# Kernel optimization log

Hardware: AMD Instinct MI355X
Metric: run time of the kernel (lower is better)

## Reference

```python
import jax, jax.numpy as jnp
import numpy as np

NUM_EMBEDDINGS = 512
EMBEDDING_DIM = 64
COMMITMENT_COST = 0.25


def setup_inputs() -> dict:
    key = jax.random.key(0)
    k1, k2 = jax.random.split(key)
    inputs = jax.random.normal(k1, (128, 1024, EMBEDDING_DIM), dtype=jnp.float32)
    embedding = jax.random.normal(k2, (NUM_EMBEDDINGS, EMBEDDING_DIM), dtype=jnp.float32)
    return {"inputs": inputs, "embedding": embedding}


def reference(inputs, embedding):
    """Eval-mode forward of VectorQuantizerEMA.

    Returns (loss, quantized, perplexity, encodings), matching the torch module
    with self.training == False.
    """
    input_shape = inputs.shape
    flat = inputs.reshape(-1, EMBEDDING_DIM)                      # [N, D]
    distances = (
        jnp.sum(flat ** 2, axis=1, keepdims=True)
        + jnp.sum(embedding ** 2, axis=1)
        - 2.0 * flat @ embedding.T
    )
    encoding_indices = jnp.argmin(distances, axis=1)              # [N]
    encodings = jax.nn.one_hot(encoding_indices, NUM_EMBEDDINGS, dtype=jnp.float32)  # [N, K]
    # quantized = onehot @ W  ==  gather rows (same math, cheaper)
    quantized = jnp.take(embedding, encoding_indices, axis=0).reshape(input_shape)

    e_latent_loss = jnp.mean((jax.lax.stop_gradient(quantized) - inputs) ** 2)
    loss = COMMITMENT_COST * e_latent_loss

    # straight-through estimator
    quantized = inputs + jax.lax.stop_gradient(quantized - inputs)

    avg_probs = jnp.mean(encodings, axis=0)                       # [K]
    perplexity = jnp.exp(-jnp.sum(avg_probs * jnp.log(avg_probs + 1e-10)))
    return loss, quantized, perplexity, encodings
```

## Files before the change

kernel.cpp:

```cpp
#include <hip/hip_runtime.h>
#include <math.h>


#define NK 512
#define ND 64
#define NROWS 131072
#define ROWS_PB 64
#define BLOCK 256
#define NBLOCKS (NROWS / ROWS_PB)
#define NTILES 32
#define XSTRIDE 68
#define MARGIN 0.02f

#define Q_OFF    1
#define PERP_OFF 8388609
#define ENC_OFF  8388610

typedef float vf2 __attribute__((ext_vector_type(2)));
typedef float vf4 __attribute__((ext_vector_type(4)));
typedef short vs8 __attribute__((ext_vector_type(8)));

__device__ __forceinline__ unsigned short bf16_rne(float v) {
    union { float f; unsigned int u; } a; a.f = v;
    return (unsigned short)((a.u + 0x7FFFu + ((a.u >> 16) & 1u)) >> 16);
}
__device__ __forceinline__ float bf16_to_f(unsigned short s) {
    union { unsigned int u; float f; } a; a.u = ((unsigned int)s) << 16;
    return a.f;
}

__global__ __launch_bounds__(64) void vq_prep(const float* __restrict__ emb,
                                              float* __restrict__ eknorm,
                                              unsigned int* __restrict__ efrag) {
    const int t = blockIdx.x;
    const int l = threadIdx.x;
    const int c = t * 16 + (l & 15);
    const int quad = l >> 4;
    #pragma unroll
    for (int f = 0; f < 4; ++f) {
        const int kbase = (f & 1) * 32 + quad * 8;
        unsigned int w[4];
        #pragma unroll
        for (int d = 0; d < 4; ++d) {
            float v0 = emb[c * ND + kbase + 2 * d];
            float v1 = emb[c * ND + kbase + 2 * d + 1];
            unsigned short h0 = bf16_rne(v0), h1 = bf16_rne(v1);
            unsigned short l0 = bf16_rne(v0 - bf16_to_f(h0));
            unsigned short l1 = bf16_rne(v1 - bf16_to_f(h1));
            unsigned short e0 = (f < 2) ? h0 : l0;
            unsigned short e1 = (f < 2) ? h1 : l1;
            w[d] = (unsigned int)e0 | ((unsigned int)e1 << 16);
        }
        unsigned int* dst = efrag + ((size_t)(t * 4 + f) * 64 + l) * 4;
        dst[0] = w[0]; dst[1] = w[1]; dst[2] = w[2]; dst[3] = w[3];
    }
    if (quad == 0) {
        const vf4* er = (const vf4*)(emb + c * ND);
        float s0 = 0.f, s1 = 0.f, s2 = 0.f, s3 = 0.f;
        #pragma unroll
        for (int j = 0; j < 16; ++j) {
            vf4 v = er[j];
            s0 += v.x * v.x; s1 += v.y * v.y; s2 += v.z * v.z; s3 += v.w * v.w;
        }
        eknorm[c] = (s0 + s1) + (s2 + s3);
    }
}

__global__ __launch_bounds__(BLOCK) void vq_main(const float* __restrict__ x,
                                                 const float* __restrict__ emb,
                                                 const float* __restrict__ eknorm,
                                                 const unsigned int* __restrict__ efrag,
                                                 float* __restrict__ out,
                                                 int* __restrict__ g_counts,
                                                 float* __restrict__ g_loss) {
    __shared__ float lds_x[ROWS_PB * XSTRIDE];
    __shared__ float ek_lds[NK];
    __shared__ float d1s[ROWS_PB], d2s[ROWS_PB];
    __shared__ int   i1s[ROWS_PB], i2s[ROWS_PB];
    __shared__ int   idx_s[ROWS_PB];
    __shared__ float red[4];

    const int tid  = threadIdx.x;
    const int wave = tid >> 6;
    const int lane = tid & 63;
    const int col  = lane & 15;
    const int quad = lane >> 4;

    {
        const vf4* xp = (const vf4*)(x + (size_t)blockIdx.x * ROWS_PB * ND);
        #pragma unroll
        for (int i = 0; i < 4; ++i) {
            int e4 = tid + i * BLOCK;
            int r  = e4 >> 4;
            int c4 = (e4 & 15) * 4;
            *(vf4*)&lds_x[r * XSTRIDE + c4] = xp[e4];
        }
        ek_lds[tid] = eknorm[tid];
        ek_lds[tid + 256] = eknorm[tid + 256];
    }
    __syncthreads();

    const int arow = wave * 16 + col;
    vs8 ah0, ah1, al0, al1;
    {
        const float* xr = &lds_x[arow * XSTRIDE];
        #pragma unroll
        for (int j = 0; j < 8; ++j) {
            float va = xr[quad * 8 + j];
            float vb = xr[32 + quad * 8 + j];
            unsigned short ha = bf16_rne(va);
            unsigned short hb = bf16_rne(vb);
            ah0[j] = (short)ha; al0[j] = (short)bf16_rne(va - bf16_to_f(ha));
            ah1[j] = (short)hb; al1[j] = (short)bf16_rne(vb - bf16_to_f(hb));
        }
    }

    float d1[4], d2[4];
    int   i1[4], i2[4];
    #pragma unroll
    for (int r = 0; r < 4; ++r) { d1[r] = INFINITY; d2[r] = INFINITY; i1[r] = 0x7FFFFFFF; i2[r] = 0x7FFFFFFF; }

    const vs8* bbase = (const vs8*)efrag;
    vs8 b0 = bbase[(0 * 4 + 0) * 64 + lane];
    vs8 b1 = bbase[(0 * 4 + 1) * 64 + lane];
    vs8 b2 = bbase[(0 * 4 + 2) * 64 + lane];
    vs8 b3 = bbase[(0 * 4 + 3) * 64 + lane];

    for (int t = 0; t < NTILES; ++t) {
        vs8 n0, n1, n2, n3;
        if (t + 1 < NTILES) {
            n0 = bbase[((t + 1) * 4 + 0) * 64 + lane];
            n1 = bbase[((t + 1) * 4 + 1) * 64 + lane];
            n2 = bbase[((t + 1) * 4 + 2) * 64 + lane];
            n3 = bbase[((t + 1) * 4 + 3) * 64 + lane];
        }
        vf4 acc = {0.f, 0.f, 0.f, 0.f};
        acc = __builtin_amdgcn_mfma_f32_16x16x32_bf16(ah0, b0, acc, 0, 0, 0);
        acc = __builtin_amdgcn_mfma_f32_16x16x32_bf16(ah1, b1, acc, 0, 0, 0);
        acc = __builtin_amdgcn_mfma_f32_16x16x32_bf16(al0, b0, acc, 0, 0, 0);
        acc = __builtin_amdgcn_mfma_f32_16x16x32_bf16(al1, b1, acc, 0, 0, 0);
        acc = __builtin_amdgcn_mfma_f32_16x16x32_bf16(ah0, b2, acc, 0, 0, 0);
        acc = __builtin_amdgcn_mfma_f32_16x16x32_bf16(ah1, b3, acc, 0, 0, 0);
        acc = __builtin_amdgcn_mfma_f32_16x16x32_bf16(al0, b2, acc, 0, 0, 0);
        acc = __builtin_amdgcn_mfma_f32_16x16x32_bf16(al1, b3, acc, 0, 0, 0);

        const float ek = ek_lds[t * 16 + col];
        const int cidx = t * 16 + col;
        #pragma unroll
        for (int r = 0; r < 4; ++r) {
            float d = ek - 2.f * acc[r];
            bool lt1 = d < d1[r];
            bool lt2 = d < d2[r];
            float nd2 = lt1 ? d1[r] : (lt2 ? d : d2[r]);
            int   ni2 = lt1 ? i1[r] : (lt2 ? cidx : i2[r]);
            d2[r] = nd2; i2[r] = ni2;
            d1[r] = lt1 ? d : d1[r];
            i1[r] = lt1 ? cidx : i1[r];
        }
        b0 = n0; b1 = n1; b2 = n2; b3 = n3;
    }

    #pragma unroll
    for (int m = 8; m >= 1; m >>= 1) {
        #pragma unroll
        for (int r = 0; r < 4; ++r) {
            float od1 = __shfl_xor(d1[r], m);
            int   oi1 = __shfl_xor(i1[r], m);
            float od2 = __shfl_xor(d2[r], m);
            int   oi2 = __shfl_xor(i2[r], m);
            bool aF = (d1[r] < od1) || (d1[r] == od1 && i1[r] < oi1);
            float n1 = aF ? d1[r] : od1;  int ni1 = aF ? i1[r] : oi1;
            float ca = aF ? od1 : d1[r];  int cia = aF ? oi1 : i1[r];
            float cb = aF ? d2[r] : od2;  int cib = aF ? i2[r] : oi2;
            bool bF = (cb < ca) || (cb == ca && cib < cia);
            float n2 = bF ? cb : ca;      int ni2 = bF ? cib : cia;
            d1[r] = n1; i1[r] = ni1; d2[r] = n2; i2[r] = ni2;
        }
    }
    if (col == 0) {
        #pragma unroll
        for (int r = 0; r < 4; ++r) {
            int lr = wave * 16 + quad * 4 + r;
            d1s[lr] = d1[r]; i1s[lr] = i1[r];
            d2s[lr] = d2[r]; i2s[lr] = i2[r];
        }
    }
    __syncthreads();

    if (tid < ROWS_PB) {
        int am = i1s[tid];
        if (d2s[tid] - d1s[tid] < MARGIN) {
            int ia = i1s[tid], ib = i2s[tid];
            const float* xr = &lds_x[tid * XSTRIDE];
            float da, db;
            {
                const vf4* er = (const vf4*)(emb + ia * ND);
                float s0 = 0.f, s1 = 0.f, s2 = 0.f, s3 = 0.f;
                #pragma unroll
                for (int j = 0; j < 16; ++j) {
                    vf4 v = er[j];
                    s0 += xr[4 * j] * v.x; s1 += xr[4 * j + 1] * v.y;
                    s2 += xr[4 * j + 2] * v.z; s3 += xr[4 * j + 3] * v.w;
                }
                da = ek_lds[ia] - 2.f * ((s0 + s1) + (s2 + s3));
            }
            {
                const vf4* er = (const vf4*)(emb + ib * ND);
                float s0 = 0.f, s1 = 0.f, s2 = 0.f, s3 = 0.f;
                #pragma unroll
                for (int j = 0; j < 16; ++j) {
                    vf4 v = er[j];
                    s0 += xr[4 * j] * v.x; s1 += xr[4 * j + 1] * v.y;
                    s2 += xr[4 * j + 2] * v.z; s3 += xr[4 * j + 3] * v.w;
                }
                db = ek_lds[ib] - 2.f * ((s0 + s1) + (s2 + s3));
            }
            am = ((db < da) || (db == da && ib < ia)) ? ib : ia;
        }
        idx_s[tid] = am;
        atomicAdd(&g_counts[am], 1);
    }
    __syncthreads();

    float lacc = 0.f;
    {
        float* qout = out + Q_OFF + (size_t)blockIdx.x * ROWS_PB * ND;
        #pragma unroll 4
        for (int i = 0; i < 16; ++i) {
            int p = tid + i * BLOCK;
            int r = p >> 6;
            int c = p & 63;
            float q = emb[idx_s[r] * ND + c];
            float xv = lds_x[r * XSTRIDE + c];
            qout[p] = q;
            float dlt = q - xv;
            lacc += dlt * dlt;
        }
    }
    #pragma unroll
    for (int off = 32; off >= 1; off >>= 1) lacc += __shfl_down(lacc, off);
    if (lane == 0) red[wave] = lacc;
    __syncthreads();
    if (tid == 0) atomicAdd(g_loss, (red[0] + red[1]) + (red[2] + red[3]));

    {
        vf2* eout = (vf2*)(out + ENC_OFF) + (size_t)blockIdx.x * ROWS_PB * NK / 2;
        #pragma unroll 4
        for (int i = 0; i < 64; ++i) {
            int p = tid + i * BLOCK;
            int r = p >> 8;
            int c2 = p & 255;
            int am = idx_s[r];
            vf2 v = {0.f, 0.f};
            if ((am >> 1) == c2) {
                if (am & 1) v.y = 1.f; else v.x = 1.f;
            }
            __builtin_nontemporal_store(v, &eout[p]);
        }
    }
}

__global__ __launch_bounds__(512) void vq_final(const int* __restrict__ g_counts,
                                                const float* __restrict__ g_loss,
                                                float* __restrict__ out) {
    __shared__ float red[8];
    int t = threadIdx.x;
    float p = (float)g_counts[t] * (1.0f / (float)NROWS);
    float h = p * logf(p + 1e-10f);
    #pragma unroll
    for (int off = 32; off >= 1; off >>= 1) h += __shfl_down(h, off);
    if ((t & 63) == 0) red[t >> 6] = h;
    __syncthreads();
    if (t == 0) {
        float s = 0.f;
        #pragma unroll
        for (int i = 0; i < 8; ++i) s += red[i];
        out[PERP_OFF] = expf(-s);
        out[0] = 0.25f * g_loss[0] / (float)(NROWS * ND);
    }
}

extern "C" void kernel_launch(void* const* d_in, const int* in_sizes, int n_in,
                              void* d_out, int out_size, void* d_ws, size_t ws_size,
                              hipStream_t stream) {
    const float* x   = (const float*)d_in[0];
    const float* emb = (const float*)d_in[1];
    float* out = (float*)d_out;

    int*          g_counts = (int*)d_ws;
    float*        g_loss   = (float*)((char*)d_ws + 2048);
    float*        eknorm   = (float*)((char*)d_ws + 4096);
    unsigned int* efrag    = (unsigned int*)((char*)d_ws + 8192);

    (void)hipMemsetAsync(d_ws, 0, 4096, stream);

    vq_prep<<<NTILES, 64, 0, stream>>>(emb, eknorm, efrag);
    vq_main<<<NBLOCKS, BLOCK, 0, stream>>>(x, emb, eknorm, efrag, out, g_counts, g_loss);
    vq_final<<<1, 512, 0, stream>>>(g_counts, g_loss, out);
}
```

Before: 372.9 us.

## Zero-fill encodings with aligned vector stores, scatter ones, drop lo×lo MFMA terms

The one-hot encodings output is now written as a bulk zero-fill of 16-byte nontemporal stores. Two 8-byte edge stores handle the misaligned output offset. After a barrier, each row's 1.0 is written in a single scatter, replacing the per-element compare-and-store loop with 8-byte stores. The distance MFMA chain drops the two low×low correction products and splits the rest over two accumulators to shorten the dependency chain. Quantized stores also become nontemporal. The precision loss from the dropped terms relies on the existing margin-based fp32 recheck. The zero-then-one ordering depends on the block barrier making global stores visible across threads.

New measurement: 392.8 us. 5.3% more time.

```diff
diff --git a/kernel.cpp b/kernel.cpp
--- a/kernel.cpp
+++ b/kernel.cpp
@@ -121,10 +121,10 @@
     for (int r = 0; r < 4; ++r) { d1[r] = INFINITY; d2[r] = INFINITY; i1[r] = 0x7FFFFFFF; i2[r] = 0x7FFFFFFF; }
 
     const vs8* bbase = (const vs8*)efrag;
-    vs8 b0 = bbase[(0 * 4 + 0) * 64 + lane];
-    vs8 b1 = bbase[(0 * 4 + 1) * 64 + lane];
-    vs8 b2 = bbase[(0 * 4 + 2) * 64 + lane];
-    vs8 b3 = bbase[(0 * 4 + 3) * 64 + lane];
+    vs8 b0 = bbase[0 * 64 + lane];
+    vs8 b1 = bbase[1 * 64 + lane];
+    vs8 b2 = bbase[2 * 64 + lane];
+    vs8 b3 = bbase[3 * 64 + lane];
 
     for (int t = 0; t < NTILES; ++t) {
         vs8 n0, n1, n2, n3;
@@ -134,21 +134,20 @@
             n2 = bbase[((t + 1) * 4 + 2) * 64 + lane];
             n3 = bbase[((t + 1) * 4 + 3) * 64 + lane];
         }
-        vf4 acc = {0.f, 0.f, 0.f, 0.f};
-        acc = __builtin_amdgcn_mfma_f32_16x16x32_bf16(ah0, b0, acc, 0, 0, 0);
-        acc = __builtin_amdgcn_mfma_f32_16x16x32_bf16(ah1, b1, acc, 0, 0, 0);
-        acc = __builtin_amdgcn_mfma_f32_16x16x32_bf16(al0, b0, acc, 0, 0, 0);
-        acc = __builtin_amdgcn_mfma_f32_16x16x32_bf16(al1, b1, acc, 0, 0, 0);
-        acc = __builtin_amdgcn_mfma_f32_16x16x32_bf16(ah0, b2, acc, 0, 0, 0);
-        acc = __builtin_amdgcn_mfma_f32_16x16x32_bf16(ah1, b3, acc, 0, 0, 0);
-        acc = __builtin_amdgcn_mfma_f32_16x16x32_bf16(al0, b2, acc, 0, 0, 0);
-        acc = __builtin_amdgcn_mfma_f32_16x16x32_bf16(al1, b3, acc, 0, 0, 0);
+        vf4 acc0 = {0.f, 0.f, 0.f, 0.f};
+        vf4 acc1 = {0.f, 0.f, 0.f, 0.f};
+        acc0 = __builtin_amdgcn_mfma_f32_16x16x32_bf16(ah0, b0, acc0, 0, 0, 0);
+        acc1 = __builtin_amdgcn_mfma_f32_16x16x32_bf16(ah1, b1, acc1, 0, 0, 0);
+        acc0 = __builtin_amdgcn_mfma_f32_16x16x32_bf16(al0, b0, acc0, 0, 0, 0);
+        acc1 = __builtin_amdgcn_mfma_f32_16x16x32_bf16(al1, b1, acc1, 0, 0, 0);
+        acc0 = __builtin_amdgcn_mfma_f32_16x16x32_bf16(ah0, b2, acc0, 0, 0, 0);
+        acc1 = __builtin_amdgcn_mfma_f32_16x16x32_bf16(ah1, b3, acc1, 0, 0, 0);
 
         const float ek = ek_lds[t * 16 + col];
         const int cidx = t * 16 + col;
         #pragma unroll
         for (int r = 0; r < 4; ++r) {
-            float d = ek - 2.f * acc[r];
+            float d = ek - 2.f * (acc0[r] + acc1[r]);
             bool lt1 = d < d1[r];
             bool lt2 = d < d2[r];
             float nd2 = lt1 ? d1[r] : (lt2 ? d : d2[r]);
@@ -183,6 +182,22 @@
             int lr = wave * 16 + quad * 4 + r;
             d1s[lr] = d1[r]; i1s[lr] = i1[r];
             d2s[lr] = d2[r]; i2s[lr] = i2[r];
+        }
+    }
+
+    float* ebase = out + ENC_OFF + (size_t)blockIdx.x * (ROWS_PB * NK);
+    {
+        if (tid == 0) {
+            vf2 z2 = {0.f, 0.f};
+            __builtin_nontemporal_store(z2, (vf2*)ebase);
+            __builtin_nontemporal_store(z2, (vf2*)(ebase + ROWS_PB * NK - 2));
+        }
+        vf4 z4 = {0.f, 0.f, 0.f, 0.f};
+        float* v4base = ebase + 2;
+        #pragma unroll 8
+        for (int i = 0; i < 32; ++i) {
+            int p = tid + i * BLOCK;
+            if (p < 8191) __builtin_nontemporal_store(z4, (vf4*)(v4base + 4 * p));
         }
     }
     __syncthreads();
@@ -232,32 +247,21 @@
             int c = p & 63;
             float q = emb[idx_s[r] * ND + c];
             float xv = lds_x[r * XSTRIDE + c];
-            qout[p] = q;
+            __builtin_nontemporal_store(q, &qout[p]);
             float dlt = q - xv;
             lacc += dlt * dlt;
         }
     }
+
+    if (tid < ROWS_PB) {
+        ebase[tid * NK + idx_s[tid]] = 1.0f;
+    }
+
     #pragma unroll
     for (int off = 32; off >= 1; off >>= 1) lacc += __shfl_down(lacc, off);
     if (lane == 0) red[wave] = lacc;
     __syncthreads();
     if (tid == 0) atomicAdd(g_loss, (red[0] + red[1]) + (red[2] + red[3]));
-
-    {
-        vf2* eout = (vf2*)(out + ENC_OFF) + (size_t)blockIdx.x * ROWS_PB * NK / 2;
-        #pragma unroll 4
-        for (int i = 0; i < 64; ++i) {
-            int p = tid + i * BLOCK;
-            int r = p >> 8;
-            int c2 = p & 255;
-            int am = idx_s[r];
-            vf2 v = {0.f, 0.f};
-            if ((am >> 1) == c2) {
-                if (am & 1) v.y = 1.f; else v.x = 1.f;
-            }
-            __builtin_nontemporal_store(v, &eout[p]);
-        }
-    }
 }
 
 __global__ __launch_bounds__(512) void vq_final(const int* __restrict__ g_counts,
```
